# Performance work log

Hardware: AMD Instinct MI355X
Metric: run time of the kernel (lower is better)

The kernel has to match this reference:

```python
import jax, jax.numpy as jnp
import numpy as np

N_HEAD = 8
D_HEAD = 64
HIDDEN = 512
T = 2048
BS = 4
SCALE = D_HEAD ** -0.5


def setup_inputs() -> dict:
    key = jax.random.key(0)
    k1, k2, k3 = jax.random.split(key, 3)
    x = jax.random.normal(k1, (BS, T, HIDDEN), dtype=jnp.float32)
    # torch Linear weight is (out,in); we store as (in,out) for x @ W
    W_qkv = jax.random.normal(k2, (HIDDEN, (2 * N_HEAD + 1) * D_HEAD), dtype=jnp.float32) * 0.02
    W_out = jax.random.normal(k3, (D_HEAD, HIDDEN), dtype=jnp.float32) * 0.02
    return {"x": x, "W_qkv": W_qkv, "W_out": W_out}


def reference(x, W_qkv, W_out):
    bs, t, h = x.shape
    qkv = x @ W_qkv  # (bs, t, (2H+1)*d)
    q, k, v = jnp.split(qkv, [N_HEAD * D_HEAD, 2 * N_HEAD * D_HEAD], axis=-1)
    q = q.reshape(bs, t, N_HEAD, D_HEAD)
    k = k.reshape(bs, t, N_HEAD, D_HEAD)
    # v is shared across heads: (bs, t, d)
    score = jnp.einsum("bqhd,bkhd->bhqk", q, k) * SCALE
    causal = jnp.triu(jnp.full((t, t), -jnp.inf, dtype=score.dtype), 1)
    score = score + causal[None, None, :, :]
    prob = jax.nn.softmax(score, axis=-1)  # (bs, H, t, t)
    attn_vec = jnp.einsum("bhqk,bkd->bhqd", prob, v)  # shared V broadcast over heads
    m_attn_vec = jnp.mean(attn_vec, axis=1)  # head-mean: (bs, t, d)
    out = m_attn_vec @ W_out  # (bs, t, hidden)
    return out, attn_vec
```

## Files before the change

kernel.cpp:

```cpp
#include <hip/hip_runtime.h>
#include <hip/hip_bf16.h>

#define NHEAD  8
#define DHEAD  64
#define HIDDEN 512
#define SEQ_T  2048
#define BATCH  4
#define NQKV   1088
#define NT     32
#define NROWS  (BATCH * SEQ_T)
#define NBH    (BATCH * NHEAD)
#define QSC    (0.125f * 1.44269504f)

typedef __attribute__((ext_vector_type(8))) short short8;
typedef __attribute__((ext_vector_type(4))) float f32x4;

__device__ __forceinline__ unsigned short f2bf(float f) {
  unsigned int u = __float_as_uint(f);
  u += 0x7FFFu + ((u >> 16) & 1u);
  return (unsigned short)(u >> 16);
}

__device__ __forceinline__ void load_lds16(const unsigned short* g, unsigned short* l) {
  __builtin_amdgcn_global_load_lds((const __attribute__((address_space(1))) void*)g,
                                   (__attribute__((address_space(3))) void*)l, 16, 0, 0);
}

#define DPPF(x, ctrl) \
  __int_as_float(__builtin_amdgcn_update_dpp(0, __float_as_int(x), (ctrl), 0xF, 0xF, true))
__device__ __forceinline__ float rsum16(float x) {
  x += DPPF(x, 0xB1);
  x += DPPF(x, 0x4E);
  x += DPPF(x, 0x141);
  x += DPPF(x, 0x140);
  return x;
}

__global__ __launch_bounds__(256) void prep(const float* __restrict__ x,
                                            const float* __restrict__ W,
                                            unsigned short* __restrict__ xb,
                                            unsigned short* __restrict__ Wt) {
  const int bx = blockIdx.x;
  const int tid = threadIdx.x;
  if (bx < 2048) {
    const size_t i0 = ((size_t)bx * 256 + tid) * 8;
    float4 a = *(const float4*)(x + i0);
    float4 b = *(const float4*)(x + i0 + 4);
    ushort4 u0, u1;
    u0.x = f2bf(a.x); u0.y = f2bf(a.y); u0.z = f2bf(a.z); u0.w = f2bf(a.w);
    u1.x = f2bf(b.x); u1.y = f2bf(b.y); u1.z = f2bf(b.z); u1.w = f2bf(b.w);
    *(ushort4*)(xb + i0) = u0;
    *(ushort4*)(xb + i0 + 4) = u1;
    return;
  }
  const int idx = bx - 2048;
  const int n0 = (idx % 17) * 64;
  const int k0 = (idx / 17) * 64;
  __shared__ float T[64 * 65];
#pragma unroll
  for (int i = 0; i < 4; ++i) {
    int f = tid + i * 256;
    int r = f >> 4;
    int c4 = (f & 15) * 4;
    float4 v = *(const float4*)(W + (size_t)(k0 + r) * NQKV + n0 + c4);
    T[r * 65 + c4 + 0] = v.x;
    T[r * 65 + c4 + 1] = v.y;
    T[r * 65 + c4 + 2] = v.z;
    T[r * 65 + c4 + 3] = v.w;
  }
  __syncthreads();
#pragma unroll
  for (int i = 0; i < 4; ++i) {
    int f = tid + i * 256;
    int n = f >> 4;
    int k4 = (f & 15) * 4;
    ushort4 u;
    u.x = f2bf(T[(k4 + 0) * 65 + n]);
    u.y = f2bf(T[(k4 + 1) * 65 + n]);
    u.z = f2bf(T[(k4 + 2) * 65 + n]);
    u.w = f2bf(T[(k4 + 3) * 65 + n]);
    *(ushort4*)(Wt + (size_t)(n0 + n) * HIDDEN + k0 + k4) = u;
  }
}

__global__ __launch_bounds__(256) void qkv_mfma(const unsigned short* __restrict__ Xb,
                                                const unsigned short* __restrict__ Wt,
                                                unsigned short* __restrict__ Y) {
  __shared__ __align__(16) unsigned short As[128 * 64];
  __shared__ __align__(16) unsigned short Bs[64 * 64];
  const int L = blockIdx.x;
  const int slot = L >> 3;
  const int bm = (L & 7) * 8 + (slot & 7);
  const int bn = slot >> 3;
  const int tid = threadIdx.x;
  const int wave = tid >> 6;
  const int lane = tid & 63;
  const int quad = lane >> 4;
  const int l15 = lane & 15;
  const int lrow = lane >> 3;
  const int lchunk = lane & 7;

  const unsigned short* xrow = Xb + (size_t)bm * 128 * HIDDEN;
  const unsigned short* wrow = Wt + (size_t)bn * 64 * HIDDEN;

  f32x4 acc[2][4];
#pragma unroll
  for (int mt = 0; mt < 2; ++mt)
#pragma unroll
    for (int nt = 0; nt < 4; ++nt) acc[mt][nt] = (f32x4){0.f, 0.f, 0.f, 0.f};

  for (int k0 = 0; k0 < HIDDEN; k0 += 64) {
    __syncthreads();
#pragma unroll
    for (int c = 0; c < 4; ++c) {
      int call = wave * 4 + c;
      int m = call * 8 + lrow;
      int clog = lchunk ^ lrow;
      load_lds16(xrow + (size_t)m * HIDDEN + k0 + clog * 8, &As[call * 512]);
    }
#pragma unroll
    for (int c = 0; c < 2; ++c) {
      int call = wave * 2 + c;
      int n = call * 8 + lrow;
      int clog = lchunk ^ lrow;
      load_lds16(wrow + (size_t)n * HIDDEN + k0 + clog * 8, &Bs[call * 512]);
    }
    __syncthreads();

#pragma unroll
    for (int ks = 0; ks < 2; ++ks) {
      short8 a[2], b[4];
#pragma unroll
      for (int mt = 0; mt < 2; ++mt) {
        int m = wave * 32 + mt * 16 + l15;
        int phys = (ks * 4 + quad) ^ (l15 & 7);
        a[mt] = *(const short8*)&As[m * 64 + phys * 8];
      }
#pragma unroll
      for (int nt = 0; nt < 4; ++nt) {
        int n = nt * 16 + l15;
        int phys = (ks * 4 + quad) ^ (l15 & 7);
        b[nt] = *(const short8*)&Bs[n * 64 + phys * 8];
      }
#pragma unroll
      for (int mt = 0; mt < 2; ++mt)
#pragma unroll
        for (int nt = 0; nt < 4; ++nt)
          acc[mt][nt] = __builtin_amdgcn_mfma_f32_16x16x32_bf16(a[mt], b[nt], acc[mt][nt], 0, 0, 0);
    }
  }

  const float qs = (bn < 8) ? QSC : 1.0f;
#pragma unroll
  for (int mt = 0; mt < 2; ++mt)
#pragma unroll
    for (int r = 0; r < 4; ++r) {
      int row = bm * 128 + wave * 32 + mt * 16 + quad * 4 + r;
#pragma unroll
      for (int nt = 0; nt < 4; ++nt) {
        int col = bn * 64 + nt * 16 + l15;
        Y[(size_t)row * NQKV + col] = f2bf(acc[mt][nt][r] * qs);
      }
    }
}

__global__ __launch_bounds__(256) void v_transpose(const unsigned short* __restrict__ qkv,
                                                   unsigned short* __restrict__ vt) {
  const int b = blockIdx.x >> 5;
  const int k0 = (blockIdx.x & 31) * 64;
  const int tid = threadIdx.x;
  __shared__ unsigned short Vs[64 * 66];

#pragma unroll
  for (int i = 0; i < 8; ++i) {
    int c = tid + i * 256;
    int row = c >> 5;
    int col2 = c & 31;
    unsigned int v = *(const unsigned int*)(qkv + (size_t)(b * SEQ_T + k0 + row) * NQKV + 1024 + col2 * 2);
    *(unsigned int*)&Vs[row * 66 + col2 * 2] = v;
  }
  __syncthreads();

#pragma unroll
  for (int i = 0; i < 16; ++i) {
    int f = tid + i * 256;
    int d = f >> 6;
    int n = f & 63;
    int c = ((n & 3) << 4) | (n >> 2);
    vt[((size_t)b * DHEAD + d) * SEQ_T + k0 + n] = Vs[c * 66 + d];
  }
}

__global__ __launch_bounds__(256, 3) void attn_pass(const unsigned short* __restrict__ qkv,
                                                    const unsigned short* __restrict__ vt,
                                                    float* __restrict__ part0,
                                                    unsigned short* __restrict__ pbuf,
                                                    float* __restrict__ lbuf) {
  const int bh = blockIdx.x;
  const int y = blockIdx.y;
  const int qt = 15 - (y >> 1);
  const int kh = y & 1;
  const int b = bh >> 3;
  const int h = bh & 7;
  const int tid = threadIdx.x;
  const int wave = tid >> 6;
  const int lane = tid & 63;
  const int quad = lane >> 4;
  const int l15 = lane & 15;

  __shared__ __align__(16) unsigned short Ks[2][64 * 64];
  __shared__ __align__(16) unsigned short Vts[2][64 * 64];
  __shared__ __align__(16) unsigned short Ps[128 * 72];

  const unsigned short* bq = qkv + (size_t)b * SEQ_T * NQKV;
  const unsigned short* bvt = vt + (size_t)b * DHEAD * SEQ_T;

  const int q0 = qt * 128;
  const int kbeg = kh ? (qt + 1) : 0;
  const int kend = kh ? (2 * qt + 1) : qt;

  short8 aq[2][2];
#pragma unroll
  for (int s = 0; s < 2; ++s) {
    const unsigned short* qp = bq + (size_t)(q0 + s * 64 + wave * 16 + l15) * NQKV + h * 64 + quad * 8;
    aq[s][0] = *(const short8*)qp;
    aq[s][1] = *(const short8*)(qp + 32);
  }

  f32x4 o[2][4];
#pragma unroll
  for (int s = 0; s < 2; ++s)
#pragma unroll
    for (int t = 0; t < 4; ++t) o[s][t] = (f32x4){0.f, 0.f, 0.f, 0.f};
  float l_part[2][4] = {{0.f, 0.f, 0.f, 0.f}, {0.f, 0.f, 0.f, 0.f}};

  const int srow = tid >> 3;
  const int sch = (tid & 7) ^ (srow & 7);
  const int ph0 = (quad ^ (l15 & 7)) * 8;

#pragma unroll
  for (int c = 0; c < 2; ++c) {
    load_lds16(bq + (size_t)(kbeg * 64 + c * 32 + srow) * NQKV + 512 + h * 64 + sch * 8,
               &Ks[0][c * 2048 + wave * 512]);
    load_lds16(bvt + (size_t)(c * 32 + srow) * SEQ_T + kbeg * 64 + sch * 8,
               &Vts[0][c * 2048 + wave * 512]);
  }

  for (int kt = kbeg; kt <= kend; ++kt) {
    const int k0 = kt * 64;
    const int cur = (kt - kbeg) & 1;
    __syncthreads();
    if (kt < kend) {
      const int kn = (kt + 1) * 64;
      const int nxt = cur ^ 1;
#pragma unroll
      for (int c = 0; c < 2; ++c) {
        load_lds16(bq + (size_t)(kn + c * 32 + srow) * NQKV + 512 + h * 64 + sch * 8,
                   &Ks[nxt][c * 2048 + wave * 512]);
        load_lds16(bvt + (size_t)(c * 32 + srow) * SEQ_T + kn + sch * 8,
                   &Vts[nxt][c * 2048 + wave * 512]);
      }
    }

    const unsigned short* ksb = Ks[cur];
    const unsigned short* vsb = Vts[cur];
    const bool needMask = (k0 + 63) > q0;

    short8 bk[4][2];
#pragma unroll
    for (int t = 0; t < 4; ++t) {
      const unsigned short* kp = &ksb[(l15 + 16 * t) * 64];
      bk[t][0] = *(const short8*)(kp + ph0);
      bk[t][1] = *(const short8*)(kp + (ph0 ^ 32));
    }

#pragma unroll
    for (int s = 0; s < 2; ++s) {
      f32x4 pr[4];
#pragma unroll
      for (int t = 0; t < 4; ++t) {
        f32x4 sv = (f32x4){0.f, 0.f, 0.f, 0.f};
        sv = __builtin_amdgcn_mfma_f32_16x16x32_bf16(aq[s][0], bk[t][0], sv, 0, 0, 0);
        sv = __builtin_amdgcn_mfma_f32_16x16x32_bf16(aq[s][1], bk[t][1], sv, 0, 0, 0);
        pr[t] = sv;
      }
      const int rbase = s * 64 + wave * 16 + quad * 4;
#pragma unroll
      for (int t = 0; t < 4; ++t)
#pragma unroll
        for (int r = 0; r < 4; ++r) {
          float p = __builtin_amdgcn_exp2f(pr[t][r]);
          if (needMask)
            p = (k0 + 16 * t + l15 <= q0 + rbase + r) ? p : 0.f;
          l_part[s][r] += p;
          pr[t][r] = p;
        }
#pragma unroll
      for (int r = 0; r < 4; ++r) {
        uint2 w;
        w.x = __builtin_amdgcn_perm(__float_as_uint(pr[1][r]), __float_as_uint(pr[0][r]), 0x07060302u);
        w.y = __builtin_amdgcn_perm(__float_as_uint(pr[3][r]), __float_as_uint(pr[2][r]), 0x07060302u);
        *(uint2*)&Ps[(rbase + r) * 72 + 4 * l15] = w;
      }
    }

    short8 bv[4][2];
#pragma unroll
    for (int t = 0; t < 4; ++t) {
      const unsigned short* vp = &vsb[(l15 + 16 * t) * 64];
      bv[t][0] = *(const short8*)(vp + ph0);
      bv[t][1] = *(const short8*)(vp + (ph0 ^ 32));
    }
    short8 ap[2][2];
#pragma unroll
    for (int s = 0; s < 2; ++s) {
      const unsigned short* pp = &Ps[(s * 64 + wave * 16 + l15) * 72];
      ap[s][0] = *(const short8*)(pp + quad * 8);
      ap[s][1] = *(const short8*)(pp + 32 + quad * 8);
    }

#pragma unroll
    for (int t = 0; t < 4; ++t)
#pragma unroll
      for (int s = 0; s < 2; ++s) {
        o[s][t] = __builtin_amdgcn_mfma_f32_16x16x32_bf16(ap[s][0], bv[t][0], o[s][t], 0, 0, 0);
        o[s][t] = __builtin_amdgcn_mfma_f32_16x16x32_bf16(ap[s][1], bv[t][1], o[s][t], 0, 0, 0);
      }
  }

#pragma unroll
  for (int s = 0; s < 2; ++s) {
#pragma unroll
    for (int r = 0; r < 4; ++r) {
      float l = rsum16(l_part[s][r]);
      const int trow = q0 + s * 64 + wave * 16 + quad * 4 + r;
      if (l15 == 0) lbuf[kh * (NBH * SEQ_T) + bh * SEQ_T + trow] = l;
      const size_t base = ((size_t)bh * SEQ_T + trow) * DHEAD;
      if (kh == 0) {
#pragma unroll
        for (int t = 0; t < 4; ++t) part0[base + l15 + 16 * t] = o[s][t][r];
      } else {
#pragma unroll
        for (int t = 0; t < 4; ++t) pbuf[base + l15 + 16 * t] = f2bf(o[s][t][r]);
      }
    }
  }
}

__global__ __launch_bounds__(256) void out_merge(const float* __restrict__ part0,
                                                 const unsigned short* __restrict__ pbuf,
                                                 const float* __restrict__ lbuf,
                                                 const float* __restrict__ Wout,
                                                 float* __restrict__ attnv,
                                                 float* __restrict__ out) {
  const int row0 = blockIdx.x * 16;
  const int tid = threadIdx.x;
  __shared__ float Ms[16][64];

#pragma unroll
  for (int i = 0; i < 4; ++i) {
    int f = tid + i * 256;
    int lr = f >> 6;
    int d = f & 63;
    int row = row0 + lr;
    int b = row >> 11;
    int t = row & 2047;
    float sum = 0.f;
#pragma unroll
    for (int hh = 0; hh < NHEAD; ++hh) {
      size_t ridx = (size_t)(b * NHEAD + hh) * SEQ_T + t;
      float inv = 1.0f / (lbuf[ridx] + lbuf[NBH * SEQ_T + ridx]);
      size_t idx = ridx * DHEAD + d;
      float m = (part0[idx] + __uint_as_float((unsigned int)pbuf[idx] << 16)) * inv;
      attnv[idx] = m;
      sum += m;
    }
    Ms[lr][d] = sum * (1.0f / NHEAD);
  }
  __syncthreads();

  const int c0 = tid * 2;
  float a0[16], a1[16];
#pragma unroll
  for (int i = 0; i < 16; ++i) { a0[i] = 0.f; a1[i] = 0.f; }

  for (int d = 0; d < 64; ++d) {
    float2 w = *(const float2*)(Wout + (size_t)d * HIDDEN + c0);
#pragma unroll
    for (int lr = 0; lr < 16; ++lr) {
      float m = Ms[lr][d];
      a0[lr] += m * w.x;
      a1[lr] += m * w.y;
    }
  }
#pragma unroll
  for (int lr = 0; lr < 16; ++lr) {
    float2 v = make_float2(a0[lr], a1[lr]);
    *(float2*)(out + (size_t)(row0 + lr) * HIDDEN + c0) = v;
  }
}

extern "C" void kernel_launch(void* const* d_in, const int* in_sizes, int n_in,
                              void* d_out, int out_size, void* d_ws, size_t ws_size,
                              hipStream_t stream) {
  const float* x     = (const float*)d_in[0];
  const float* W_qkv = (const float*)d_in[1];
  const float* W_out = (const float*)d_in[2];

  float* out      = (float*)d_out;
  float* attn_vec = out + (size_t)BATCH * SEQ_T * HIDDEN;

  unsigned short* qkv = (unsigned short*)d_ws;
  unsigned short* vt  = qkv + (size_t)NROWS * NQKV;
  unsigned short* xb  = vt + (size_t)BATCH * DHEAD * SEQ_T;
  unsigned short* Wt  = xb + (size_t)NROWS * HIDDEN;
  unsigned short* pbuf = xb;
  float*          lbuf = (float*)Wt;

  prep<<<dim3(2048 + 136), 256, 0, stream>>>(x, W_qkv, xb, Wt);
  qkv_mfma<<<dim3(64 * 17), 256, 0, stream>>>(xb, Wt, qkv);
  v_transpose<<<dim3(BATCH * NT), 256, 0, stream>>>(qkv, vt);
  attn_pass<<<dim3(NBH, 32), 256, 0, stream>>>(qkv, vt, attn_vec, pbuf, lbuf);
  out_merge<<<dim3(512), 256, 0, stream>>>(attn_vec, pbuf, lbuf, W_out, attn_vec, out);
}
```

Baseline: 147.4 us.

## Widen QKV GEMM tile to 128 columns and store both attention partials as bf16

The QKV GEMM now computes 128x128 tiles instead of 128x64, with the output pitch padded to 1152 columns and the extra weight rows zero-filled in prep. This halves the block count and raises MFMA work per LDS load, at the cost of some wasted compute on padding. Both key-half partial outputs of attention are now written as bf16 to separate buffers instead of one fp32 and one bf16, and the merge kernel reads them with vectorised ushort4 loads and writes float4. This cuts write and read traffic for the partials but adds a little rounding error to the first half.

```diff
diff --git a/kernel.cpp b/kernel.cpp
--- a/kernel.cpp
+++ b/kernel.cpp
@@ -7,6 +7,7 @@
 #define SEQ_T  2048
 #define BATCH  4
 #define NQKV   1088
+#define QPITCH 1152
 #define NT     32
 #define NROWS  (BATCH * SEQ_T)
 #define NBH    (BATCH * NHEAD)
@@ -19,6 +20,9 @@
   unsigned int u = __float_as_uint(f);
   u += 0x7FFFu + ((u >> 16) & 1u);
   return (unsigned short)(u >> 16);
+}
+__device__ __forceinline__ float bf2f(unsigned short u) {
+  return __uint_as_float((unsigned int)u << 16);
 }
 
 __device__ __forceinline__ void load_lds16(const unsigned short* g, unsigned short* l) {
@@ -53,6 +57,14 @@
     *(ushort4*)(xb + i0 + 4) = u1;
     return;
   }
+  if (bx >= 2184) {
+    const int z = bx - 2184;
+    const size_t base = (size_t)NQKV * HIDDEN + ((size_t)z * 256 + tid) * 16;
+    uint4 zero = {0u, 0u, 0u, 0u};
+    *(uint4*)(Wt + base) = zero;
+    *(uint4*)(Wt + base + 8) = zero;
+    return;
+  }
   const int idx = bx - 2048;
   const int n0 = (idx % 17) * 64;
   const int k0 = (idx / 17) * 64;
@@ -83,11 +95,11 @@
   }
 }
 
-__global__ __launch_bounds__(256) void qkv_mfma(const unsigned short* __restrict__ Xb,
-                                                const unsigned short* __restrict__ Wt,
-                                                unsigned short* __restrict__ Y) {
+__global__ __launch_bounds__(256, 3) void qkv_mfma(const unsigned short* __restrict__ Xb,
+                                                   const unsigned short* __restrict__ Wt,
+                                                   unsigned short* __restrict__ Y) {
   __shared__ __align__(16) unsigned short As[128 * 64];
-  __shared__ __align__(16) unsigned short Bs[64 * 64];
+  __shared__ __align__(16) unsigned short Bs[128 * 64];
   const int L = blockIdx.x;
   const int slot = L >> 3;
   const int bm = (L & 7) * 8 + (slot & 7);
@@ -101,13 +113,13 @@
   const int lchunk = lane & 7;
 
   const unsigned short* xrow = Xb + (size_t)bm * 128 * HIDDEN;
-  const unsigned short* wrow = Wt + (size_t)bn * 64 * HIDDEN;
-
-  f32x4 acc[2][4];
+  const unsigned short* wrow = Wt + (size_t)bn * 128 * HIDDEN;
+
+  f32x4 acc[2][8];
 #pragma unroll
   for (int mt = 0; mt < 2; ++mt)
 #pragma unroll
-    for (int nt = 0; nt < 4; ++nt) acc[mt][nt] = (f32x4){0.f, 0.f, 0.f, 0.f};
+    for (int nt = 0; nt < 8; ++nt) acc[mt][nt] = (f32x4){0.f, 0.f, 0.f, 0.f};
 
   for (int k0 = 0; k0 < HIDDEN; k0 += 64) {
     __syncthreads();
@@ -117,19 +129,13 @@
       int m = call * 8 + lrow;
       int clog = lchunk ^ lrow;
       load_lds16(xrow + (size_t)m * HIDDEN + k0 + clog * 8, &As[call * 512]);
-    }
-#pragma unroll
-    for (int c = 0; c < 2; ++c) {
-      int call = wave * 2 + c;
-      int n = call * 8 + lrow;
-      int clog = lchunk ^ lrow;
-      load_lds16(wrow + (size_t)n * HIDDEN + k0 + clog * 8, &Bs[call * 512]);
+      load_lds16(wrow + (size_t)m * HIDDEN + k0 + clog * 8, &Bs[call * 512]);
     }
     __syncthreads();
 
 #pragma unroll
     for (int ks = 0; ks < 2; ++ks) {
-      short8 a[2], b[4];
+      short8 a[2], b[8];
 #pragma unroll
       for (int mt = 0; mt < 2; ++mt) {
         int m = wave * 32 + mt * 16 + l15;
@@ -137,7 +143,7 @@
         a[mt] = *(const short8*)&As[m * 64 + phys * 8];
       }
 #pragma unroll
-      for (int nt = 0; nt < 4; ++nt) {
+      for (int nt = 0; nt < 8; ++nt) {
         int n = nt * 16 + l15;
         int phys = (ks * 4 + quad) ^ (l15 & 7);
         b[nt] = *(const short8*)&Bs[n * 64 + phys * 8];
@@ -145,21 +151,21 @@
 #pragma unroll
       for (int mt = 0; mt < 2; ++mt)
 #pragma unroll
-        for (int nt = 0; nt < 4; ++nt)
+        for (int nt = 0; nt < 8; ++nt)
           acc[mt][nt] = __builtin_amdgcn_mfma_f32_16x16x32_bf16(a[mt], b[nt], acc[mt][nt], 0, 0, 0);
     }
   }
 
-  const float qs = (bn < 8) ? QSC : 1.0f;
+  const float qs = (bn < 4) ? QSC : 1.0f;
 #pragma unroll
   for (int mt = 0; mt < 2; ++mt)
 #pragma unroll
     for (int r = 0; r < 4; ++r) {
       int row = bm * 128 + wave * 32 + mt * 16 + quad * 4 + r;
 #pragma unroll
-      for (int nt = 0; nt < 4; ++nt) {
-        int col = bn * 64 + nt * 16 + l15;
-        Y[(size_t)row * NQKV + col] = f2bf(acc[mt][nt][r] * qs);
+      for (int nt = 0; nt < 8; ++nt) {
+        int col = bn * 128 + nt * 16 + l15;
+        Y[(size_t)row * QPITCH + col] = f2bf(acc[mt][nt][r] * qs);
       }
     }
 }
@@ -176,7 +182,7 @@
     int c = tid + i * 256;
     int row = c >> 5;
     int col2 = c & 31;
-    unsigned int v = *(const unsigned int*)(qkv + (size_t)(b * SEQ_T + k0 + row) * NQKV + 1024 + col2 * 2);
+    unsigned int v = *(const unsigned int*)(qkv + (size_t)(b * SEQ_T + k0 + row) * QPITCH + 1024 + col2 * 2);
     *(unsigned int*)&Vs[row * 66 + col2 * 2] = v;
   }
   __syncthreads();
@@ -193,8 +199,8 @@
 
 __global__ __launch_bounds__(256, 3) void attn_pass(const unsigned short* __restrict__ qkv,
                                                     const unsigned short* __restrict__ vt,
-                                                    float* __restrict__ part0,
-                                                    unsigned short* __restrict__ pbuf,
+                                                    unsigned short* __restrict__ pbuf0,
+                                                    unsigned short* __restrict__ pbuf1,
                                                     float* __restrict__ lbuf) {
   const int bh = blockIdx.x;
   const int y = blockIdx.y;
@@ -212,7 +218,7 @@
   __shared__ __align__(16) unsigned short Vts[2][64 * 64];
   __shared__ __align__(16) unsigned short Ps[128 * 72];
 
-  const unsigned short* bq = qkv + (size_t)b * SEQ_T * NQKV;
+  const unsigned short* bq = qkv + (size_t)b * SEQ_T * QPITCH;
   const unsigned short* bvt = vt + (size_t)b * DHEAD * SEQ_T;
 
   const int q0 = qt * 128;
@@ -222,7 +228,7 @@
   short8 aq[2][2];
 #pragma unroll
   for (int s = 0; s < 2; ++s) {
-    const unsigned short* qp = bq + (size_t)(q0 + s * 64 + wave * 16 + l15) * NQKV + h * 64 + quad * 8;
+    const unsigned short* qp = bq + (size_t)(q0 + s * 64 + wave * 16 + l15) * QPITCH + h * 64 + quad * 8;
     aq[s][0] = *(const short8*)qp;
     aq[s][1] = *(const short8*)(qp + 32);
   }
@@ -240,7 +246,7 @@
 
 #pragma unroll
   for (int c = 0; c < 2; ++c) {
-    load_lds16(bq + (size_t)(kbeg * 64 + c * 32 + srow) * NQKV + 512 + h * 64 + sch * 8,
+    load_lds16(bq + (size_t)(kbeg * 64 + c * 32 + srow) * QPITCH + 512 + h * 64 + sch * 8,
                &Ks[0][c * 2048 + wave * 512]);
     load_lds16(bvt + (size_t)(c * 32 + srow) * SEQ_T + kbeg * 64 + sch * 8,
                &Vts[0][c * 2048 + wave * 512]);
@@ -255,7 +261,7 @@
       const int nxt = cur ^ 1;
 #pragma unroll
       for (int c = 0; c < 2; ++c) {
-        load_lds16(bq + (size_t)(kn + c * 32 + srow) * NQKV + 512 + h * 64 + sch * 8,
+        load_lds16(bq + (size_t)(kn + c * 32 + srow) * QPITCH + 512 + h * 64 + sch * 8,
                    &Ks[nxt][c * 2048 + wave * 512]);
         load_lds16(bvt + (size_t)(c * 32 + srow) * SEQ_T + kn + sch * 8,
                    &Vts[nxt][c * 2048 + wave * 512]);
@@ -328,6 +334,7 @@
       }
   }
 
+  unsigned short* pb = kh ? pbuf1 : pbuf0;
 #pragma unroll
   for (int s = 0; s < 2; ++s) {
 #pragma unroll
@@ -336,19 +343,14 @@
       const int trow = q0 + s * 64 + wave * 16 + quad * 4 + r;
       if (l15 == 0) lbuf[kh * (NBH * SEQ_T) + bh * SEQ_T + trow] = l;
       const size_t base = ((size_t)bh * SEQ_T + trow) * DHEAD;
-      if (kh == 0) {
-#pragma unroll
-        for (int t = 0; t < 4; ++t) part0[base + l15 + 16 * t] = o[s][t][r];
-      } else {
-#pragma unroll
-        for (int t = 0; t < 4; ++t) pbuf[base + l15 + 16 * t] = f2bf(o[s][t][r]);
-      }
-    }
-  }
-}
-
-__global__ __launch_bounds__(256) void out_merge(const float* __restrict__ part0,
-                                                 const unsigned short* __restrict__ pbuf,
+#pragma unroll
+      for (int t = 0; t < 4; ++t) pb[base + l15 + 16 * t] = f2bf(o[s][t][r]);
+    }
+  }
+}
+
+__global__ __launch_bounds__(256) void out_merge(const unsigned short* __restrict__ pbuf0,
+                                                 const unsigned short* __restrict__ pbuf1,
                                                  const float* __restrict__ lbuf,
                                                  const float* __restrict__ Wout,
                                                  float* __restrict__ attnv,
@@ -357,25 +359,32 @@
   const int tid = threadIdx.x;
   __shared__ float Ms[16][64];
 
-#pragma unroll
-  for (int i = 0; i < 4; ++i) {
-    int f = tid + i * 256;
-    int lr = f >> 6;
-    int d = f & 63;
-    int row = row0 + lr;
-    int b = row >> 11;
-    int t = row & 2047;
-    float sum = 0.f;
+  {
+    const int lr = tid >> 4;
+    const int d0 = (tid & 15) * 4;
+    const int row = row0 + lr;
+    const int b = row >> 11;
+    const int t = row & 2047;
+    float s0 = 0.f, s1 = 0.f, s2 = 0.f, s3 = 0.f;
 #pragma unroll
     for (int hh = 0; hh < NHEAD; ++hh) {
-      size_t ridx = (size_t)(b * NHEAD + hh) * SEQ_T + t;
-      float inv = 1.0f / (lbuf[ridx] + lbuf[NBH * SEQ_T + ridx]);
-      size_t idx = ridx * DHEAD + d;
-      float m = (part0[idx] + __uint_as_float((unsigned int)pbuf[idx] << 16)) * inv;
-      attnv[idx] = m;
-      sum += m;
-    }
-    Ms[lr][d] = sum * (1.0f / NHEAD);
+      const size_t ridx = (size_t)(b * NHEAD + hh) * SEQ_T + t;
+      const float inv = 1.0f / (lbuf[ridx] + lbuf[NBH * SEQ_T + ridx]);
+      const size_t idx = ridx * DHEAD + d0;
+      ushort4 A = *(const ushort4*)(pbuf0 + idx);
+      ushort4 B = *(const ushort4*)(pbuf1 + idx);
+      float4 m;
+      m.x = (bf2f(A.x) + bf2f(B.x)) * inv;
+      m.y = (bf2f(A.y) + bf2f(B.y)) * inv;
+      m.z = (bf2f(A.z) + bf2f(B.z)) * inv;
+      m.w = (bf2f(A.w) + bf2f(B.w)) * inv;
+      *(float4*)(attnv + idx) = m;
+      s0 += m.x; s1 += m.y; s2 += m.z; s3 += m.w;
+    }
+    Ms[lr][d0 + 0] = s0 * 0.125f;
+    Ms[lr][d0 + 1] = s1 * 0.125f;
+    Ms[lr][d0 + 2] = s2 * 0.125f;
+    Ms[lr][d0 + 3] = s3 * 0.125f;
   }
   __syncthreads();
 
@@ -410,16 +419,17 @@
   float* out      = (float*)d_out;
   float* attn_vec = out + (size_t)BATCH * SEQ_T * HIDDEN;
 
-  unsigned short* qkv = (unsigned short*)d_ws;
-  unsigned short* vt  = qkv + (size_t)NROWS * NQKV;
-  unsigned short* xb  = vt + (size_t)BATCH * DHEAD * SEQ_T;
-  unsigned short* Wt  = xb + (size_t)NROWS * HIDDEN;
-  unsigned short* pbuf = xb;
-  float*          lbuf = (float*)Wt;
-
-  prep<<<dim3(2048 + 136), 256, 0, stream>>>(x, W_qkv, xb, Wt);
-  qkv_mfma<<<dim3(64 * 17), 256, 0, stream>>>(xb, Wt, qkv);
+  unsigned short* qkv  = (unsigned short*)d_ws;
+  unsigned short* vt   = qkv + (size_t)NROWS * QPITCH;
+  unsigned short* xb   = vt + (size_t)BATCH * DHEAD * SEQ_T;
+  unsigned short* Wt   = xb + (size_t)NROWS * HIDDEN;
+  unsigned short* pbuf0 = Wt + (size_t)QPITCH * HIDDEN;
+  unsigned short* pbuf1 = pbuf0 + (size_t)NBH * SEQ_T * DHEAD;
+  float*          lbuf  = (float*)(pbuf1 + (size_t)NBH * SEQ_T * DHEAD);
+
+  prep<<<dim3(2048 + 136 + 8), 256, 0, stream>>>(x, W_qkv, xb, Wt);
+  qkv_mfma<<<dim3(576), 256, 0, stream>>>(xb, Wt, qkv);
   v_transpose<<<dim3(BATCH * NT), 256, 0, stream>>>(qkv, vt);
-  attn_pass<<<dim3(NBH, 32), 256, 0, stream>>>(qkv, vt, attn_vec, pbuf, lbuf);
-  out_merge<<<dim3(512), 256, 0, stream>>>(attn_vec, pbuf, lbuf, W_out, attn_vec, out);
-}
+  attn_pass<<<dim3(NBH, 32), 256, 0, stream>>>(qkv, vt, pbuf0, pbuf1, lbuf);
+  out_merge<<<dim3(512), 256, 0, stream>>>(pbuf0, pbuf1, lbuf, W_out, attn_vec, out);
+}
```

Measured after the change: 140.9 us. 1.05x faster.
